# Performance work log

Measured on AMD Instinct MI355X. Metric: run time of the kernel, lower is better.

Reference implementation:

```python
import jax, jax.numpy as jnp
import numpy as np

NSIDE = 128
LMAX = 4 * NSIDE - 1            # nlat = 511 (lmax default)
MMAX = (4 * NSIDE) // 2 + 1     # nlon//2 + 1 = 257
NPIX = 12 * NSIDE * NSIDE       # 196608 HEALPix pixels
PAD = 8 * NSIDE                 # Bluestein padding (power of two >= 2*max nphi)


def _ring_geometry(nside):
    """Static HEALPix ring layout: pixels per ring, ring offsets, phi of pixel 0."""
    ntheta = 4 * nside - 1
    t = np.arange(ntheta)
    nphi = np.where(t < nside - 1, 4 * (t + 1),
           np.where(t <= 3 * nside - 1, 4 * nside, 4 * (4 * nside - 1 - t))).astype(np.int64)
    cum = np.concatenate([[0], np.cumsum(nphi)[:-1]]).astype(np.int64)
    phi0 = np.empty(ntheta)
    for tt in range(ntheta):
        if nside - 1 <= tt <= 3 * nside - 1:      # equatorial belt
            shift = 0.5 * ((tt - nside + 2) % 2)
            factor = np.pi / (2 * nside)
        elif tt + 1 > 3 * nside:                  # south polar cap
            shift = 0.5
            factor = np.pi / (2 * (4 * nside - tt - 1))
        else:                                     # north polar cap
            shift = 0.5
            factor = np.pi / (2 * (tt + 1))
        phi0[tt] = factor * shift
    return nphi, cum, phi0


def setup_inputs() -> dict:
    key = jax.random.key(0)
    k1, k2, k3 = jax.random.split(key, 3)
    x_re = jax.random.normal(k1, (LMAX, MMAX), jnp.float32)
    x_im = jax.random.normal(k2, (LMAX, MMAX), jnp.float32)
    # pct stands in for the precomputed associated-Legendre table (mmax, lmax, nlat)
    pct = jax.random.normal(k3, (MMAX, LMAX, LMAX), jnp.float32) * 0.02
    return {"x_re": x_re, "x_im": x_im, "pct": pct}


def reference(x_re, x_im, pct):
    nside = NSIDE
    L = pct.shape[0]                     # mmax
    nphi, cum, phi0 = _ring_geometry(nside)
    n = np.arange(PAD)

    # inverse Legendre transform: ftm[k, m] = sum_l x[l, m] * pct[m, l, k]
    rl = jnp.einsum('lm,mlk->km', x_re, pct)
    im = jnp.einsum('lm,mlk->km', x_im, pct)
    ftm = (rl + 1j * im).astype(jnp.complex64)            # (ntheta, L)

    # per-ring phase shift exp(i*m*phi_ring_offset)  (static chirp)
    phase = np.exp(1j * np.arange(L)[None, :] * phi0[:, None]).astype(np.complex64)
    ftm = ftm * phase

    # conjugated hermitian extension of each ring spectrum to length nphi (zero padded to PAD)
    half = nphi // 2 + 1
    head = n[None, :] < half[:, None]
    in_ring = n[None, :] < nphi[:, None]
    idx = np.where(head, n[None, :], nphi[:, None] - n[None, :])
    valid = in_ring & (idx >= 0) & (idx < L)
    idx_c = np.clip(idx, 0, L - 1)
    g = jnp.take_along_axis(ftm, jnp.asarray(idx_c), axis=1)  # (ntheta, PAD)
    fm_full = jnp.where(valid, jnp.where(jnp.asarray(head), jnp.conj(g), g), 0.0)

    # Bluestein chirps (static, per-ring modulus nphi)
    coef = np.pi * n[None, :] ** 2 / nphi[:, None]
    chirp_a = np.where(in_ring, np.exp(1j * coef), 0).astype(np.complex64)
    chirp_b = np.where(in_ring, np.exp(-1j * coef), 0).astype(np.complex64)
    tail = n[None, :] >= PAD - nphi[:, None] + 1
    tail_coef = np.pi * (PAD - n[None, :]) ** 2 / nphi[:, None]
    y_pad = chirp_a + np.where(tail, np.exp(1j * tail_coef), 0).astype(np.complex64)

    # chirp-z via circular convolution: batched over all rings at once
    x_pad = fm_full * jnp.asarray(chirp_b)
    conv = jnp.fft.ifft(jnp.fft.fft(x_pad, axis=-1) * jnp.fft.fft(jnp.asarray(y_pad), axis=-1), axis=-1)
    vals = jnp.real(conv * jnp.asarray(chirp_b))          # (ntheta, PAD)

    # scatter ring values into the flat HEALPix map (out-of-ring slots -> dump index NPIX)
    pix = np.where(in_ring, cum[:, None] + n[None, :], NPIX).reshape(-1)
    f = jnp.zeros(NPIX + 1, jnp.float32).at[jnp.asarray(pix)].set(vals.reshape(-1).astype(jnp.float32))
    return f[:NPIX]
```

## Files before the change

kernel.cpp:

```cpp
#include <hip/hip_runtime.h>
#include <math.h>

#ifndef M_PI
#define M_PI 3.14159265358979323846
#endif

#define NSIDE  128
#define NTHETA 511
#define MMAX   257
#define NPIX   196608

__global__ __launch_bounds__(256)
void ftm_kernel(const float* __restrict__ x_re,
                const float* __restrict__ x_im,
                const float* __restrict__ pct,
                float* __restrict__ ftm_re,
                float* __restrict__ ftm_im)
{
    __shared__ float xr[NTHETA];
    __shared__ float xi[NTHETA];
    const int m   = blockIdx.y;
    const int tid = threadIdx.x;
    for (int i = tid; i < NTHETA; i += 256) {
        xr[i] = x_re[(size_t)i * MMAX + m];
        xi[i] = x_im[(size_t)i * MMAX + m];
    }
    __syncthreads();
    const int k = blockIdx.x * 256 + tid;
    if (k >= NTHETA) return;

    const float* p = pct + (size_t)m * NTHETA * NTHETA + k;
    float ar = 0.f, ai = 0.f;
    int l = 0;
    for (; l <= NTHETA - 8; l += 8) {
        float v[8];
        #pragma unroll
        for (int u = 0; u < 8; ++u) v[u] = p[(size_t)(l + u) * NTHETA];
        #pragma unroll
        for (int u = 0; u < 8; ++u) {
            ar = fmaf(xr[l + u], v[u], ar);
            ai = fmaf(xi[l + u], v[u], ai);
        }
    }
    for (; l < NTHETA; ++l) {
        float v = p[(size_t)l * NTHETA];
        ar = fmaf(xr[l], v, ar);
        ai = fmaf(xi[l], v, ai);
    }
    ftm_re[(size_t)k * MMAX + m] = ar;
    ftm_im[(size_t)k * MMAX + m] = ai;
}

__global__ __launch_bounds__(256)
void ring_kernel(const float* __restrict__ ftm_re,
                 const float* __restrict__ ftm_im,
                 float* __restrict__ out)
{
    const int t = blockIdx.y;
    int nphi, cum;
    double phi0;
    if (t < NSIDE - 1) {
        nphi = 4 * (t + 1);
        cum  = 2 * t * (t + 1);
        phi0 = M_PI / (4.0 * (t + 1));
    } else if (t <= 3 * NSIDE - 1) {
        nphi = 4 * NSIDE;
        cum  = 2 * (NSIDE - 1) * NSIDE + (t - (NSIDE - 1)) * 4 * NSIDE;
        phi0 = (M_PI / (2.0 * NSIDE)) * (0.5 * (double)((t - NSIDE + 2) % 2));
    } else {
        int s = 4 * NSIDE - 1 - t;
        nphi = 4 * s;
        cum  = NPIX - 2 * s * (s + 1);
        phi0 = M_PI / (4.0 * s);
    }
    if ((int)blockIdx.x * 256 >= nphi) return;

    const int mtop = nphi / 2;
    __shared__ float fr[MMAX];
    __shared__ float fi[MMAX];
    for (int i = threadIdx.x; i <= mtop; i += 256) {
        fr[i] = ftm_re[(size_t)t * MMAX + i];
        fi[i] = ftm_im[(size_t)t * MMAX + i];
    }
    __syncthreads();

    const int k = blockIdx.x * 256 + threadIdx.x;
    if (k >= nphi) return;

    double phi = phi0 + (2.0 * M_PI) * ((double)k / (double)nphi);
    float sp, cp;
    sincosf((float)phi, &sp, &cp);

    float cr = 1.f, ci = 0.f;
    float acc = fr[0];
    for (int m = 1; m < mtop; ++m) {
        float nr = cr * cp - ci * sp;
        float ni = cr * sp + ci * cp;
        cr = nr; ci = ni;
        acc += 2.f * (fr[m] * cr - fi[m] * ci);
    }
    {
        float nr = cr * cp - ci * sp;
        float ni = cr * sp + ci * cp;
        acc += fr[mtop] * nr - fi[mtop] * ni;
    }
    out[cum + k] = acc;
}

extern "C" void kernel_launch(void* const* d_in, const int* in_sizes, int n_in,
                              void* d_out, int out_size, void* d_ws, size_t ws_size,
                              hipStream_t stream)
{
    const float* x_re = (const float*)d_in[0];
    const float* x_im = (const float*)d_in[1];
    const float* pct  = (const float*)d_in[2];
    float* out = (float*)d_out;

    float* ftm_re = (float*)d_ws;
    float* ftm_im = ftm_re + (size_t)NTHETA * MMAX;

    ftm_kernel<<<dim3(2, MMAX), 256, 0, stream>>>(x_re, x_im, pct, ftm_re, ftm_im);
    ring_kernel<<<dim3(2, NTHETA), 256, 0, stream>>>(ftm_re, ftm_im, out);
}
```

Measured before the change: 70.03 us.

## Skip unused Legendre columns, split l-reduction into chunks with LDS double buffering

For each m, the Legendre kernel now reads and computes only the output rings k in [klo, NTHETA-klo). The ring synthesis never reads ftm entries with m above nphi/2, so the skipped entries are never used, and this cuts streamed pct bytes by roughly a quarter. The l reduction is split into 4 chunks of 128 rows, one per block. Each block stages pct rows into a double-buffered LDS tile with float2 loads, and small and large m are paired for load balance. The ring kernel sums the 4 partial ftm buffers, which adds extra workspace and some extra reads in exchange.

```diff
diff --git a/kernel.cpp b/kernel.cpp
--- a/kernel.cpp
+++ b/kernel.cpp
@@ -9,52 +9,114 @@
 #define NTHETA 511
 #define MMAX   257
 #define NPIX   196608
+#define PCT_M  ((size_t)NTHETA * NTHETA)
+#define MN     ((size_t)NTHETA * MMAX)
+#define NCH    4
+#define GROWS  8
+#define NGRP   16
 
-__global__ __launch_bounds__(256)
+__global__ __launch_bounds__(256, 4)
 void ftm_kernel(const float* __restrict__ x_re,
                 const float* __restrict__ x_im,
                 const float* __restrict__ pct,
-                float* __restrict__ ftm_re,
-                float* __restrict__ ftm_im)
+                float* __restrict__ ftm_p)
 {
-    __shared__ float xr[NTHETA];
-    __shared__ float xi[NTHETA];
-    const int m   = blockIdx.y;
+    const int q    = blockIdx.x >> 3;
+    const int r    = blockIdx.x & 7;
+    const int pick = r & 1;
+    if (q == 128 && pick) return;
+    const int m = pick ? 256 - q : q;
+    const int j = r >> 1;
+
+    const int klo   = (m >= 2) ? ((m + 1) >> 1) - 1 : 0;
+    const int cnt   = NTHETA - 2 * klo;
+    const int l0    = j * 128;
+    const int nrows = min(128, NTHETA - l0);
+    const int nT    = (cnt + 2) >> 1;
+
+    __shared__ float2 xs[128];
+    __shared__ float  tile[2][GROWS][512];
+
     const int tid = threadIdx.x;
-    for (int i = tid; i < NTHETA; i += 256) {
-        xr[i] = x_re[(size_t)i * MMAX + m];
-        xi[i] = x_im[(size_t)i * MMAX + m];
+    if (tid < nrows) {
+        int l = l0 + tid;
+        xs[tid] = make_float2(x_re[(size_t)l * MMAX + m],
+                              x_im[(size_t)l * MMAX + m]);
     }
+
+    const int par = (m + klo + l0) & 1;
+    const bool loader = (tid < nT);
+
+    float a0r = 0.f, a0i = 0.f, a1r = 0.f, a1i = 0.f;
+    float2 st[GROWS];
+
+    #define LOADG(g)                                                         \
+        _Pragma("unroll")                                                    \
+        for (int rr = 0; rr < GROWS; ++rr) {                                 \
+            int row = (g) * GROWS + rr;                                      \
+            bool ok = (row < nrows) && loader;                               \
+            size_t A  = (size_t)m * PCT_M +                                  \
+                        (size_t)(l0 + (ok ? row : 0)) * NTHETA + klo;        \
+            size_t A8 = A & ~(size_t)1;                                      \
+            st[rr] = ok ? *(const float2*)(pct + A8 + 2 * tid)               \
+                        : make_float2(0.f, 0.f);                             \
+        }
+
+    #define WRITEG(g, buf)                                                   \
+        _Pragma("unroll")                                                    \
+        for (int rr = 0; rr < GROWS; ++rr) {                                 \
+            int row = (g) * GROWS + rr;                                      \
+            if (row < nrows && loader)                                       \
+                *(float2*)&tile[buf][rr][2 * tid] = st[rr];                  \
+        }
+
+    #define CONSUMEG(g, buf)                                                 \
+        _Pragma("unroll")                                                    \
+        for (int rr = 0; rr < GROWS; ++rr) {                                 \
+            int row = (g) * GROWS + rr;                                      \
+            if (row < nrows) {                                               \
+                int s2 = (par + row) & 1;                                    \
+                float2 xv = xs[row];                                         \
+                float v0 = tile[buf][rr][tid + s2];                          \
+                int i1 = (tid + 256 < cnt) ? (tid + 256 + s2) : s2;          \
+                float v1 = tile[buf][rr][i1];                                \
+                a0r = fmaf(xv.x, v0, a0r);  a0i = fmaf(xv.y, v0, a0i);       \
+                a1r = fmaf(xv.x, v1, a1r);  a1i = fmaf(xv.y, v1, a1i);       \
+            }                                                                \
+        }
+
+    LOADG(0);
+    WRITEG(0, 0);
     __syncthreads();
-    const int k = blockIdx.x * 256 + tid;
-    if (k >= NTHETA) return;
+    int buf = 0;
+    for (int g = 0; g < NGRP; ++g) {
+        if (g + 1 < NGRP) { LOADG(g + 1); }
+        CONSUMEG(g, buf);
+        if (g + 1 < NGRP) {
+            WRITEG(g + 1, buf ^ 1);
+            __syncthreads();
+        }
+        buf ^= 1;
+    }
 
-    const float* p = pct + (size_t)m * NTHETA * NTHETA + k;
-    float ar = 0.f, ai = 0.f;
-    int l = 0;
-    for (; l <= NTHETA - 8; l += 8) {
-        float v[8];
-        #pragma unroll
-        for (int u = 0; u < 8; ++u) v[u] = p[(size_t)(l + u) * NTHETA];
-        #pragma unroll
-        for (int u = 0; u < 8; ++u) {
-            ar = fmaf(xr[l + u], v[u], ar);
-            ai = fmaf(xi[l + u], v[u], ai);
-        }
+    float* base = ftm_p + (size_t)j * 2 * MN;
+    const int k0 = klo + tid;
+    if (tid < cnt) {
+        base[(size_t)k0 * MMAX + m]      = a0r;
+        base[MN + (size_t)k0 * MMAX + m] = a0i;
     }
-    for (; l < NTHETA; ++l) {
-        float v = p[(size_t)l * NTHETA];
-        ar = fmaf(xr[l], v, ar);
-        ai = fmaf(xi[l], v, ai);
+    if (tid + 256 < cnt) {
+        const int k1 = k0 + 256;
+        base[(size_t)k1 * MMAX + m]      = a1r;
+        base[MN + (size_t)k1 * MMAX + m] = a1i;
     }
-    ftm_re[(size_t)k * MMAX + m] = ar;
-    ftm_im[(size_t)k * MMAX + m] = ai;
+    #undef LOADG
+    #undef WRITEG
+    #undef CONSUMEG
 }
 
 __global__ __launch_bounds__(256)
-void ring_kernel(const float* __restrict__ ftm_re,
-                 const float* __restrict__ ftm_im,
-                 float* __restrict__ out)
+void ring_kernel(const float* __restrict__ ftm_p, float* __restrict__ out)
 {
     const int t = blockIdx.y;
     int nphi, cum;
@@ -79,8 +141,14 @@
     __shared__ float fr[MMAX];
     __shared__ float fi[MMAX];
     for (int i = threadIdx.x; i <= mtop; i += 256) {
-        fr[i] = ftm_re[(size_t)t * MMAX + i];
-        fi[i] = ftm_im[(size_t)t * MMAX + i];
+        size_t o = (size_t)t * MMAX + i;
+        float sr = 0.f, si = 0.f;
+        #pragma unroll
+        for (int p = 0; p < NCH; ++p) {
+            sr += ftm_p[(size_t)p * 2 * MN + o];
+            si += ftm_p[(size_t)p * 2 * MN + MN + o];
+        }
+        fr[i] = sr;  fi[i] = si;
     }
     __syncthreads();
 
@@ -93,11 +161,11 @@
 
     float cr = 1.f, ci = 0.f;
     float acc = fr[0];
-    for (int m = 1; m < mtop; ++m) {
+    for (int mm = 1; mm < mtop; ++mm) {
         float nr = cr * cp - ci * sp;
         float ni = cr * sp + ci * cp;
         cr = nr; ci = ni;
-        acc += 2.f * (fr[m] * cr - fi[m] * ci);
+        acc += 2.f * (fr[mm] * cr - fi[mm] * ci);
     }
     {
         float nr = cr * cp - ci * sp;
@@ -116,9 +184,8 @@
     const float* pct  = (const float*)d_in[2];
     float* out = (float*)d_out;
 
-    float* ftm_re = (float*)d_ws;
-    float* ftm_im = ftm_re + (size_t)NTHETA * MMAX;
+    float* ftm_p = (float*)d_ws;
 
-    ftm_kernel<<<dim3(2, MMAX), 256, 0, stream>>>(x_re, x_im, pct, ftm_re, ftm_im);
-    ring_kernel<<<dim3(2, NTHETA), 256, 0, stream>>>(ftm_re, ftm_im, out);
+    ftm_kernel<<<dim3(129 * 8), 256, 0, stream>>>(x_re, x_im, pct, ftm_p);
+    ring_kernel<<<dim3(2, NTHETA), 256, 0, stream>>>(ftm_p, out);
 }
```

Measured after the change: 67.46 us. -3.7%, faster.

## Skip unused Legendre rows per m and split the l-reduction across blocks

Applied to the files above, without the earlier changes.

The Legendre-transform kernel now computes ftm only for ring indices k whose ring actually uses order m (k in [ceil(m/2)-1, NTHETA-that)), so it reads less of the pct table. The l-sum is split into 8 chunks of 64 so more blocks run in parallel. Each block handles the pair m and 256-m to balance the triangular workload. Partial sums go to an m-major workspace and are reduced while the ring kernel loads them, which adds extra workspace traffic and 8x more reads in the ring kernel's staging loop.

```diff
diff --git a/kernel.cpp b/kernel.cpp
--- a/kernel.cpp
+++ b/kernel.cpp
@@ -9,52 +9,76 @@
 #define NTHETA 511
 #define MMAX   257
 #define NPIX   196608
+#define PCT_M  ((size_t)NTHETA * NTHETA)
+#define MN     ((size_t)MMAX * NTHETA)
+#define NCH    8
 
 __global__ __launch_bounds__(256)
 void ftm_kernel(const float* __restrict__ x_re,
                 const float* __restrict__ x_im,
                 const float* __restrict__ pct,
-                float* __restrict__ ftm_re,
-                float* __restrict__ ftm_im)
+                float* __restrict__ ftm_p)
 {
-    __shared__ float xr[NTHETA];
-    __shared__ float xi[NTHETA];
-    const int m   = blockIdx.y;
+    const int q   = blockIdx.x >> 3;
+    const int lc  = blockIdx.x & 7;
+    const int l0  = lc * 64;
     const int tid = threadIdx.x;
-    for (int i = tid; i < NTHETA; i += 256) {
-        xr[i] = x_re[(size_t)i * MMAX + m];
-        xi[i] = x_im[(size_t)i * MMAX + m];
+    const int nr  = min(64, NTHETA - l0);
+
+    __shared__ float2 xs[2][64];
+    if (tid < 128) {
+        const int side = tid >> 6, rr = tid & 63;
+        const int m = side ? 256 - q : q;
+        const int l = l0 + rr;
+        float2 v = make_float2(0.f, 0.f);
+        if (l < NTHETA)
+            v = make_float2(x_re[(size_t)l * MMAX + m],
+                            x_im[(size_t)l * MMAX + m]);
+        xs[side][rr] = v;
     }
     __syncthreads();
-    const int k = blockIdx.x * 256 + tid;
-    if (k >= NTHETA) return;
 
-    const float* p = pct + (size_t)m * NTHETA * NTHETA + k;
-    float ar = 0.f, ai = 0.f;
-    int l = 0;
-    for (; l <= NTHETA - 8; l += 8) {
-        float v[8];
-        #pragma unroll
-        for (int u = 0; u < 8; ++u) v[u] = p[(size_t)(l + u) * NTHETA];
-        #pragma unroll
-        for (int u = 0; u < 8; ++u) {
-            ar = fmaf(xr[l + u], v[u], ar);
-            ai = fmaf(xi[l + u], v[u], ai);
+    for (int side = 0; side < 2; ++side) {
+        if (side && q == 128) break;
+        const int m   = side ? 256 - q : q;
+        const int klo = (m >= 2) ? ((m + 1) >> 1) - 1 : 0;
+        const int cnt = NTHETA - 2 * klo;
+        const int k0  = klo + tid;
+        const bool has2 = (tid + 256) < cnt;
+        const int k1  = k0 + 256;
+
+        const float* p = pct + (size_t)m * PCT_M + (size_t)l0 * NTHETA;
+        float a0r = 0.f, a0i = 0.f, a1r = 0.f, a1i = 0.f;
+
+        for (int b = 0; b < 8; ++b) {
+            float v0[8], v1[8];
+            #pragma unroll
+            for (int u = 0; u < 8; ++u) {
+                int rr = b * 8 + u;
+                int rc = rr < nr ? rr : nr - 1;
+                v0[u] = p[(size_t)rc * NTHETA + k0];
+                v1[u] = has2 ? p[(size_t)rc * NTHETA + k1] : 0.f;
+            }
+            #pragma unroll
+            for (int u = 0; u < 8; ++u) {
+                float2 xv = xs[side][b * 8 + u];
+                a0r = fmaf(xv.x, v0[u], a0r);  a0i = fmaf(xv.y, v0[u], a0i);
+                a1r = fmaf(xv.x, v1[u], a1r);  a1i = fmaf(xv.y, v1[u], a1i);
+            }
+        }
+
+        float* P = ftm_p + (size_t)lc * 2 * MN;
+        P[(size_t)m * NTHETA + k0]      = a0r;
+        P[MN + (size_t)m * NTHETA + k0] = a0i;
+        if (has2) {
+            P[(size_t)m * NTHETA + k1]      = a1r;
+            P[MN + (size_t)m * NTHETA + k1] = a1i;
         }
     }
-    for (; l < NTHETA; ++l) {
-        float v = p[(size_t)l * NTHETA];
-        ar = fmaf(xr[l], v, ar);
-        ai = fmaf(xi[l], v, ai);
-    }
-    ftm_re[(size_t)k * MMAX + m] = ar;
-    ftm_im[(size_t)k * MMAX + m] = ai;
 }
 
 __global__ __launch_bounds__(256)
-void ring_kernel(const float* __restrict__ ftm_re,
-                 const float* __restrict__ ftm_im,
-                 float* __restrict__ out)
+void ring_kernel(const float* __restrict__ ftm_p, float* __restrict__ out)
 {
     const int t = blockIdx.y;
     int nphi, cum;
@@ -79,8 +103,14 @@
     __shared__ float fr[MMAX];
     __shared__ float fi[MMAX];
     for (int i = threadIdx.x; i <= mtop; i += 256) {
-        fr[i] = ftm_re[(size_t)t * MMAX + i];
-        fi[i] = ftm_im[(size_t)t * MMAX + i];
+        const size_t o = (size_t)i * NTHETA + t;
+        float sr = 0.f, si = 0.f;
+        #pragma unroll
+        for (int p = 0; p < NCH; ++p) {
+            sr += ftm_p[(size_t)p * 2 * MN + o];
+            si += ftm_p[(size_t)p * 2 * MN + MN + o];
+        }
+        fr[i] = sr;  fi[i] = si;
     }
     __syncthreads();
 
@@ -93,11 +123,11 @@
 
     float cr = 1.f, ci = 0.f;
     float acc = fr[0];
-    for (int m = 1; m < mtop; ++m) {
+    for (int mm = 1; mm < mtop; ++mm) {
         float nr = cr * cp - ci * sp;
         float ni = cr * sp + ci * cp;
         cr = nr; ci = ni;
-        acc += 2.f * (fr[m] * cr - fi[m] * ci);
+        acc += 2.f * (fr[mm] * cr - fi[mm] * ci);
     }
     {
         float nr = cr * cp - ci * sp;
@@ -116,9 +146,8 @@
     const float* pct  = (const float*)d_in[2];
     float* out = (float*)d_out;
 
-    float* ftm_re = (float*)d_ws;
-    float* ftm_im = ftm_re + (size_t)NTHETA * MMAX;
+    float* ftm_p = (float*)d_ws;
 
-    ftm_kernel<<<dim3(2, MMAX), 256, 0, stream>>>(x_re, x_im, pct, ftm_re, ftm_im);
-    ring_kernel<<<dim3(2, NTHETA), 256, 0, stream>>>(ftm_re, ftm_im, out);
+    ftm_kernel<<<dim3(129 * NCH), 256, 0, stream>>>(x_re, x_im, pct, ftm_p);
+    ring_kernel<<<dim3(2, NTHETA), 256, 0, stream>>>(ftm_p, out);
 }
```

Measured after the change: 67.43 us. 1.04x faster.
